# Optimization experiments

Hardware: AMD Instinct MI355X
Metric: run time of the kernel (lower is better)

## Reference

```python
import jax, jax.numpy as jnp
import numpy as np

N = 100000   # nodes
E = 1600000  # edges
G = 512      # graphs in batch
F_IN = 128
H = 128
F_OUT = 1


def setup_inputs() -> dict:
    key = jax.random.key(0)
    ks = jax.random.split(key, 12)
    x = jax.random.normal(ks[0], (N, F_IN), dtype=jnp.float32)
    src = jax.random.randint(ks[1], (E,), 0, N, dtype=jnp.int32)
    dst = jax.random.randint(ks[2], (E,), 0, N, dtype=jnp.int32)
    node2graph = jnp.sort(jax.random.randint(ks[3], (N,), 0, G, dtype=jnp.int32))
    s_in = 1.0 / np.sqrt(F_IN)
    s_h = 1.0 / np.sqrt(H)
    W0 = jax.random.normal(ks[4], (F_IN, H), dtype=jnp.float32) * s_in
    b0 = jnp.zeros((H,), dtype=jnp.float32)
    W1 = jax.random.normal(ks[5], (H, H), dtype=jnp.float32) * s_h
    b1 = jnp.zeros((H,), dtype=jnp.float32)
    W2 = jax.random.normal(ks[6], (H, H), dtype=jnp.float32) * s_h
    b2 = jnp.zeros((H,), dtype=jnp.float32)
    Wm1 = jax.random.normal(ks[7], (H, H), dtype=jnp.float32) * s_h
    bm1 = jnp.zeros((H,), dtype=jnp.float32)
    Wm2 = jax.random.normal(ks[8], (H, F_OUT), dtype=jnp.float32) * s_h
    bm2 = jnp.zeros((F_OUT,), dtype=jnp.float32)
    return {"x": x, "src": src, "dst": dst, "node2graph": node2graph,
            "W0": W0, "b0": b0, "W1": W1, "b1": b1, "W2": W2, "b2": b2,
            "Wm1": Wm1, "bm1": bm1, "Wm2": Wm2, "bm2": bm2}


def _degree_norms(src, dst):
    ones = jnp.ones((E,), dtype=jnp.float32)
    out_deg = jax.ops.segment_sum(ones, src, num_segments=N)
    in_deg = jax.ops.segment_sum(ones, dst, num_segments=N)
    norm_out = jax.lax.rsqrt(jnp.maximum(out_deg, 1.0))  # [N]
    norm_in = jax.lax.rsqrt(jnp.maximum(in_deg, 1.0))    # [N]
    return norm_out, norm_in


def _graph_conv(x, src, dst, norm_out, norm_in, W, b):
    # DGL GraphConv, norm='both', in_feats <= out_feats path:
    # aggregate normalized src features, then linear + activation.
    xs = x * norm_out[:, None]
    msg = xs[src]                                         # [E, H] gather
    agg = jax.ops.segment_sum(msg, dst, num_segments=N)   # [N, H] scatter-add
    agg = agg * norm_in[:, None]
    return jax.nn.relu(agg @ W + b)


def reference(x, src, dst, node2graph, W0, b0, W1, b1, W2, b2, Wm1, bm1, Wm2, bm2):
    norm_out, norm_in = _degree_norms(src, dst)
    h = _graph_conv(x, src, dst, norm_out, norm_in, W0, b0)
    h = _graph_conv(h, src, dst, norm_out, norm_in, W1, b1)
    h = _graph_conv(h, src, dst, norm_out, norm_in, W2, b2)
    # sum_nodes readout per graph
    g = jax.ops.segment_sum(h, node2graph, num_segments=G)  # [G, H]
    # MLP head: Linear -> ReLU -> Linear
    return jax.nn.relu(g @ Wm1 + bm1) @ Wm2 + bm2           # [G, 1]
```

## Files before the change

### kernel.cpp

```cpp
#include <hip/hip_runtime.h>

#define NN 100000
#define NE 1600000
#define NG 512
#define HD 128

#define NBK 196
#define CHUNK 5120
#define NC 313
#define LH (2 * NBK * NC)

typedef _Float16 half4 __attribute__((ext_vector_type(4)));
typedef _Float16 h8 __attribute__((ext_vector_type(8)));
typedef float f32x4 __attribute__((ext_vector_type(4)));

__global__ __launch_bounds__(256) void k_hist(const int* __restrict__ src,
                                              const int* __restrict__ dst,
                                              int* __restrict__ H) {
    __shared__ int hd[NBK], hs[NBK];
    int c = blockIdx.x;
    for (int i = threadIdx.x; i < NBK; i += 256) { hd[i] = 0; hs[i] = 0; }
    __syncthreads();
    int e0 = c * CHUNK;
    int e1 = e0 + CHUNK; if (e1 > NE) e1 = NE;
    for (int e = e0 + threadIdx.x; e < e1; e += 256) {
        atomicAdd(&hd[dst[e] >> 9], 1);
        atomicAdd(&hs[src[e] >> 9], 1);
    }
    __syncthreads();
    for (int i = threadIdx.x; i < NBK; i += 256) {
        H[i * NC + c] = hd[i];
        H[NBK * NC + i * NC + c] = hs[i];
    }
}

__global__ __launch_bounds__(256) void k_scan1g(int* __restrict__ H,
                                                int* __restrict__ bsum, int L) {
    __shared__ int s[256];
    int i = blockIdx.x * 256 + threadIdx.x;
    int v = (i < L) ? H[i] : 0;
    s[threadIdx.x] = v;
    __syncthreads();
    for (int off = 1; off < 256; off <<= 1) {
        int t = (threadIdx.x >= off) ? s[threadIdx.x - off] : 0;
        __syncthreads();
        s[threadIdx.x] += t;
        __syncthreads();
    }
    if (i < L) H[i] = s[threadIdx.x] - v;
    if (threadIdx.x == 255) bsum[blockIdx.x] = s[255];
}

__global__ __launch_bounds__(512) void k_scan2(int* __restrict__ bsum, int nb) {
    __shared__ int s[512];
    int v = (threadIdx.x < nb) ? bsum[threadIdx.x] : 0;
    s[threadIdx.x] = v;
    __syncthreads();
    for (int off = 1; off < 512; off <<= 1) {
        int t = (threadIdx.x >= off) ? s[threadIdx.x - off] : 0;
        __syncthreads();
        s[threadIdx.x] += t;
        __syncthreads();
    }
    if (threadIdx.x < nb) bsum[threadIdx.x] = s[threadIdx.x] - v;
}

__global__ __launch_bounds__(256) void k_scan3g(int* __restrict__ H,
                                                const int* __restrict__ bsum, int L) {
    int i = blockIdx.x * 256 + threadIdx.x;
    if (i < L) H[i] += bsum[i >> 8];
}

__global__ __launch_bounds__(256) void k_scatter(const int* __restrict__ src,
                                                 const int* __restrict__ dst,
                                                 const int* __restrict__ H,
                                                 int2* __restrict__ dpart,
                                                 int* __restrict__ spart) {
    __shared__ int cd[NBK], cs[NBK];
    int c = blockIdx.x;
    for (int i = threadIdx.x; i < NBK; i += 256) {
        cd[i] = H[i * NC + c];
        cs[i] = H[NBK * NC + i * NC + c] - NE;
    }
    __syncthreads();
    int e0 = c * CHUNK;
    int e1 = e0 + CHUNK; if (e1 > NE) e1 = NE;
    for (int e = e0 + threadIdx.x; e < e1; e += 256) {
        int s = src[e], d = dst[e];
        int pd = atomicAdd(&cd[d >> 9], 1);
        dpart[pd] = make_int2(s, d);
        int ps = atomicAdd(&cs[s >> 9], 1);
        spart[ps] = s;
    }
}

__global__ __launch_bounds__(256) void k_bucket(const int2* __restrict__ dpart,
                                                const int* __restrict__ spart,
                                                const int* __restrict__ H,
                                                int* __restrict__ offs,
                                                int* __restrict__ csr,
                                                float* __restrict__ ni,
                                                float* __restrict__ no) {
    __shared__ int deg[512];
    __shared__ int cur[512];
    __shared__ int tmp[256];
    int b = blockIdx.x;
    bool isDst = (b < NBK);
    int bb = isDst ? b : b - NBK;
    int start, end;
    if (isDst) {
        start = H[bb * NC];
        end = (bb + 1 < NBK) ? H[(bb + 1) * NC] : NE;
    } else {
        start = H[NBK * NC + bb * NC] - NE;
        end = (bb + 1 < NBK) ? H[NBK * NC + (bb + 1) * NC] - NE : NE;
    }
    for (int i = threadIdx.x; i < 512; i += 256) deg[i] = 0;
    __syncthreads();
    if (isDst) {
        for (int i = start + threadIdx.x; i < end; i += 256)
            atomicAdd(&deg[dpart[i].y & 511], 1);
    } else {
        for (int i = start + threadIdx.x; i < end; i += 256)
            atomicAdd(&deg[spart[i] & 511], 1);
    }
    __syncthreads();
    int vb = bb * 512;
    if (!isDst) {
        for (int i = threadIdx.x; i < 512; i += 256) {
            int v = vb + i;
            if (v < NN) no[v] = rsqrtf(fmaxf((float)deg[i], 1.0f));
        }
        return;
    }
    int t = threadIdx.x;
    int a0 = deg[2 * t], a1 = deg[2 * t + 1];
    int pair = a0 + a1;
    tmp[t] = pair;
    __syncthreads();
    for (int off = 1; off < 256; off <<= 1) {
        int v2 = (t >= off) ? tmp[t - off] : 0;
        __syncthreads();
        tmp[t] += v2;
        __syncthreads();
    }
    int ex = tmp[t] - pair;
    cur[2 * t] = start + ex;
    cur[2 * t + 1] = start + ex + a0;
    __syncthreads();
    for (int i = threadIdx.x; i < 512; i += 256) {
        int v = vb + i;
        if (v < NN) {
            offs[v] = cur[i];
            ni[v] = rsqrtf(fmaxf((float)deg[i], 1.0f));
        }
    }
    if (b == NBK - 1 && threadIdx.x == 0) offs[NN] = NE;
    __syncthreads();
    for (int i = start + threadIdx.x; i < end; i += 256) {
        int2 e = dpart[i];
        int p = atomicAdd(&cur[e.y & 511], 1);
        csr[p] = e.x;
    }
}

__global__ __launch_bounds__(256) void k_castw(const float* __restrict__ W0,
                                               const float* __restrict__ W1,
                                               const float* __restrict__ W2,
                                               _Float16* __restrict__ Bt) {
    int i = blockIdx.x * 256 + threadIdx.x;
    if (i >= 3 * 16384) return;
    int w = i >> 14;
    int rem = i & 16383;
    int n = rem >> 7;
    int k = rem & 127;
    const float* W = (w == 0) ? W0 : ((w == 1) ? W1 : W2);
    Bt[i] = (_Float16)W[k * 128 + n];
}

template <typename TA>
__global__ __launch_bounds__(256) void k_gemm_mfma(const TA* __restrict__ A,
                                                   const _Float16* __restrict__ Bt,
                                                   const float* __restrict__ no,
                                                   _Float16* __restrict__ Zh,
                                                   int nrows) {
    __shared__ _Float16 Bs[128 * 136];
    int tid = threadIdx.x;
    {
        const h8* B8 = (const h8*)Bt;
        h8* Bs8 = (h8*)Bs;
        for (int i = tid; i < 2048; i += 256) {
            int n = i >> 4, c = i & 15;
            Bs8[n * 17 + c] = B8[i];
        }
    }

    int wave = tid >> 6;
    int lane = tid & 63;
    int m16 = lane & 15;
    int quad = lane >> 4;
    int rowbase = blockIdx.x * 64 + wave * 16;
    int row = rowbase + m16;
    bool valid = row < nrows;

    h8 afrag[4];
    if (valid) {
        if constexpr (sizeof(TA) == 2) {
            const h8* Arow = (const h8*)(A + (size_t)row * 128);
#pragma unroll
            for (int kk = 0; kk < 4; kk++) afrag[kk] = Arow[kk * 4 + quad];
        } else {
            const float4* Arow = (const float4*)(A + (size_t)row * 128);
#pragma unroll
            for (int kk = 0; kk < 4; kk++) {
                float4 lo = Arow[kk * 8 + quad * 2];
                float4 hi = Arow[kk * 8 + quad * 2 + 1];
                h8 a;
                a[0] = (_Float16)lo.x; a[1] = (_Float16)lo.y;
                a[2] = (_Float16)lo.z; a[3] = (_Float16)lo.w;
                a[4] = (_Float16)hi.x; a[5] = (_Float16)hi.y;
                a[6] = (_Float16)hi.z; a[7] = (_Float16)hi.w;
                afrag[kk] = a;
            }
        }
    } else {
#pragma unroll
        for (int kk = 0; kk < 4; kk++) {
            h8 a;
#pragma unroll
            for (int j = 0; j < 8; j++) a[j] = (_Float16)0.f;
            afrag[kk] = a;
        }
    }

    __syncthreads();

    f32x4 acc[8];
#pragma unroll
    for (int nt = 0; nt < 8; nt++) acc[nt] = (f32x4){0.f, 0.f, 0.f, 0.f};

    const h8* Bs8 = (const h8*)Bs;
#pragma unroll
    for (int nt = 0; nt < 8; nt++) {
        const h8* Bp = Bs8 + (size_t)(nt * 16 + m16) * 17;
#pragma unroll
        for (int kk = 0; kk < 4; kk++) {
            acc[nt] = __builtin_amdgcn_mfma_f32_16x16x32_f16(afrag[kk], Bp[kk * 4 + quad],
                                                             acc[nt], 0, 0, 0);
        }
    }

    float nor[4];
#pragma unroll
    for (int r = 0; r < 4; r++) {
        int grow = rowbase + quad * 4 + r;
        nor[r] = (grow < nrows) ? no[grow] : 0.f;
    }

    __syncthreads();
    {
        int lr0 = wave * 16 + quad * 4;
#pragma unroll
        for (int nt = 0; nt < 8; nt++) {
#pragma unroll
            for (int r = 0; r < 4; r++) {
                Bs[(size_t)(lr0 + r) * 136 + nt * 16 + m16] =
                    (_Float16)(acc[nt][r] * nor[r]);
            }
        }
    }
    __syncthreads();

    int blockrow0 = blockIdx.x * 64;
    for (int i = tid; i < 1024; i += 256) {
        int r = i >> 4, cch = i & 15;
        int grow = blockrow0 + r;
        if (grow < nrows) {
            h8 val = *(const h8*)&Bs[(size_t)r * 136 + cch * 8];
            *(h8*)&Zh[(size_t)grow * 128 + cch * 8] = val;
        }
    }
}

__global__ __launch_bounds__(128) void k_agg(const h8* __restrict__ Zh,
                                             const int* __restrict__ offs,
                                             const int* __restrict__ csr,
                                             const float* __restrict__ ni,
                                             const float* __restrict__ b,
                                             h8* __restrict__ H16) {
    int v = blockIdx.x * 8 + (threadIdx.x >> 4);
    int c = threadIdx.x & 15;
    int s = offs[v];
    int e = offs[v + 1];
    float a0[8], a1[8];
#pragma unroll
    for (int j = 0; j < 8; j++) { a0[j] = 0.f; a1[j] = 0.f; }
    int i = s;
    for (; i + 4 <= e; i += 4) {
        int u0 = csr[i];
        int u1 = csr[i + 1];
        int u2 = csr[i + 2];
        int u3 = csr[i + 3];
        h8 z0 = Zh[(size_t)u0 * 16 + c];
        h8 z1 = Zh[(size_t)u1 * 16 + c];
        h8 z2 = Zh[(size_t)u2 * 16 + c];
        h8 z3 = Zh[(size_t)u3 * 16 + c];
#pragma unroll
        for (int j = 0; j < 8; j++) {
            a0[j] += (float)z0[j] + (float)z1[j];
            a1[j] += (float)z2[j] + (float)z3[j];
        }
    }
    for (; i < e; i++) {
        int u = csr[i];
        h8 z = Zh[(size_t)u * 16 + c];
#pragma unroll
        for (int j = 0; j < 8; j++) a0[j] += (float)z[j];
    }
    float niv = ni[v];
    const float* bb = b + c * 8;
    h8 r;
#pragma unroll
    for (int j = 0; j < 8; j++)
        r[j] = (_Float16)fmaxf((a0[j] + a1[j]) * niv + bb[j], 0.f);
    H16[(size_t)v * 16 + c] = r;
}

__global__ __launch_bounds__(128) void k_readout(const h8* __restrict__ H8,
                                                 const int* __restrict__ n2g,
                                                 float* __restrict__ g) {
    __shared__ float red[128 * 8];
    int gi = blockIdx.x;
    int t = threadIdx.x;
    int slot = t >> 4;
    int c = t & 15;

    int lo = 0, hi = NN;
    while (lo < hi) { int mid = (lo + hi) >> 1; if (n2g[mid] < gi) lo = mid + 1; else hi = mid; }
    int s = lo;
    hi = NN;
    while (lo < hi) { int mid = (lo + hi) >> 1; if (n2g[mid] < gi + 1) lo = mid + 1; else hi = mid; }
    int e = lo;

    float acc[8];
#pragma unroll
    for (int j = 0; j < 8; j++) acc[j] = 0.f;
    for (int v = s + slot; v < e; v += 8) {
        h8 z = H8[(size_t)v * 16 + c];
#pragma unroll
        for (int j = 0; j < 8; j++) acc[j] += (float)z[j];
    }
#pragma unroll
    for (int j = 0; j < 8; j++) red[t * 8 + j] = acc[j];
    __syncthreads();
    for (int off = 4; off >= 1; off >>= 1) {
        if (slot < off) {
#pragma unroll
            for (int j = 0; j < 8; j++)
                red[t * 8 + j] += red[(t + off * 16) * 8 + j];
        }
        __syncthreads();
    }
    if (slot == 0) {
#pragma unroll
        for (int j = 0; j < 8; j++)
            g[gi * 128 + c * 8 + j] = red[t * 8 + j];
    }
}

__global__ __launch_bounds__(128) void k_head(const float* __restrict__ g,
                                              const float* __restrict__ Wm1,
                                              const float* __restrict__ bm1,
                                              const float* __restrict__ Wm2,
                                              const float* __restrict__ bm2,
                                              float* __restrict__ out) {
    __shared__ float gs[128];
    __shared__ float red[128];
    int gi = blockIdx.x;
    int f = threadIdx.x;
    gs[f] = g[gi * 128 + f];
    __syncthreads();
    float acc = bm1[f];
    for (int k = 0; k < 128; k++) acc += gs[k] * Wm1[k * 128 + f];
    float h1 = fmaxf(acc, 0.f);
    red[f] = h1 * Wm2[f];
    __syncthreads();
    for (int s2 = 64; s2 > 0; s2 >>= 1) {
        if (f < s2) red[f] += red[f + s2];
        __syncthreads();
    }
    if (f == 0) out[gi] = red[0] + bm2[0];
}

extern "C" void kernel_launch(void* const* d_in, const int* in_sizes, int n_in,
                              void* d_out, int out_size, void* d_ws, size_t ws_size,
                              hipStream_t stream) {
    const float* x   = (const float*)d_in[0];
    const int*   src = (const int*)d_in[1];
    const int*   dst = (const int*)d_in[2];
    const int*   n2g = (const int*)d_in[3];
    const float* W0  = (const float*)d_in[4];
    const float* b0  = (const float*)d_in[5];
    const float* W1  = (const float*)d_in[6];
    const float* b1  = (const float*)d_in[7];
    const float* W2  = (const float*)d_in[8];
    const float* b2  = (const float*)d_in[9];
    const float* Wm1 = (const float*)d_in[10];
    const float* bm1 = (const float*)d_in[11];
    const float* Wm2 = (const float*)d_in[12];
    const float* bm2 = (const float*)d_in[13];
    float* out = (float*)d_out;

    char* p = (char*)d_ws;
    auto carve = [&](size_t bytes) -> char* {
        char* r = p;
        p += (bytes + 255) & ~(size_t)255;
        return r;
    };
    _Float16* zh  = (_Float16*)carve((size_t)NN * HD * 2);
    _Float16* h16 = (_Float16*)carve((size_t)NN * HD * 2);
    _Float16* Bt  = (_Float16*)carve((size_t)3 * 128 * 128 * 2);
    float* no     = (float*)carve((size_t)NN * 4);
    float* ni     = (float*)carve((size_t)NN * 4);
    int*   offs   = (int*)carve((size_t)(NN + 1) * 4);
    int*   csr    = (int*)carve((size_t)NE * 4);
    int*   Hh     = (int*)carve((size_t)LH * 4);
    int*   bsum   = (int*)carve((size_t)512 * 4);
    int2*  dpart  = (int2*)carve((size_t)NE * 8);
    int*   spart  = (int*)carve((size_t)NE * 4);
    float* g      = (float*)carve((size_t)NG * HD * 4);

    k_castw<<<(3 * 16384 + 255) / 256, 256, 0, stream>>>(W0, W1, W2, Bt);

    int scan_blocks = (LH + 255) / 256;
    k_hist<<<NC, 256, 0, stream>>>(src, dst, Hh);
    k_scan1g<<<scan_blocks, 256, 0, stream>>>(Hh, bsum, LH);
    k_scan2<<<1, 512, 0, stream>>>(bsum, scan_blocks);
    k_scan3g<<<scan_blocks, 256, 0, stream>>>(Hh, bsum, LH);
    k_scatter<<<NC, 256, 0, stream>>>(src, dst, Hh, dpart, spart);
    k_bucket<<<2 * NBK, 256, 0, stream>>>(dpart, spart, Hh, offs, csr, ni, no);

    int gemm_blocks = (NN + 63) / 64;

    k_gemm_mfma<float><<<gemm_blocks, 256, 0, stream>>>(x, Bt, no, zh, NN);
    k_agg<<<NN / 8, 128, 0, stream>>>((const h8*)zh, offs, csr, ni, b0, (h8*)h16);
    k_gemm_mfma<_Float16><<<gemm_blocks, 256, 0, stream>>>(h16, Bt + 16384, no, zh, NN);
    k_agg<<<NN / 8, 128, 0, stream>>>((const h8*)zh, offs, csr, ni, b1, (h8*)h16);
    k_gemm_mfma<_Float16><<<gemm_blocks, 256, 0, stream>>>(h16, Bt + 32768, no, zh, NN);
    k_agg<<<NN / 8, 128, 0, stream>>>((const h8*)zh, offs, csr, ni, b2, (h8*)h16);

    k_readout<<<NG, 128, 0, stream>>>((const h8*)h16, n2g, g);
    k_head<<<NG, 128, 0, stream>>>(g, Wm1, bm1, Wm2, bm2, out);
}
```

Measured before the change: 417.6 us.

## Pack partition entries into narrower ints and persist B fragments in GEMM registers

The scatter/bucket stage now packs each dst-partition entry into one 32-bit int (17-bit source plus 9-bit local dst), and stores the src partition as 16-bit local indices. This halves or more the traffic of the CSR-build intermediates. The GEMM kernel loads all B fragments into registers once and loops over four 64-row tiles per block. Each wave writes its own rows through LDS without block-wide syncs, so B staging is amortised over more rows. The cost is much higher register pressure (128 h8 B regs per lane), which may reduce occupancy.

Measured after the change: 420.5 us. About the same (+0.7%).

```diff
diff --git a/kernel.cpp b/kernel.cpp
--- a/kernel.cpp
+++ b/kernel.cpp
@@ -74,8 +74,8 @@
 __global__ __launch_bounds__(256) void k_scatter(const int* __restrict__ src,
                                                  const int* __restrict__ dst,
                                                  const int* __restrict__ H,
-                                                 int2* __restrict__ dpart,
-                                                 int* __restrict__ spart) {
+                                                 int* __restrict__ dpart,
+                                                 unsigned short* __restrict__ spart) {
     __shared__ int cd[NBK], cs[NBK];
     int c = blockIdx.x;
     for (int i = threadIdx.x; i < NBK; i += 256) {
@@ -88,14 +88,14 @@
     for (int e = e0 + threadIdx.x; e < e1; e += 256) {
         int s = src[e], d = dst[e];
         int pd = atomicAdd(&cd[d >> 9], 1);
-        dpart[pd] = make_int2(s, d);
+        dpart[pd] = s | ((d & 511) << 17);
         int ps = atomicAdd(&cs[s >> 9], 1);
-        spart[ps] = s;
-    }
-}
-
-__global__ __launch_bounds__(256) void k_bucket(const int2* __restrict__ dpart,
-                                                const int* __restrict__ spart,
+        spart[ps] = (unsigned short)(s & 511);
+    }
+}
+
+__global__ __launch_bounds__(256) void k_bucket(const int* __restrict__ dpart,
+                                                const unsigned short* __restrict__ spart,
                                                 const int* __restrict__ H,
                                                 int* __restrict__ offs,
                                                 int* __restrict__ csr,
@@ -119,10 +119,10 @@
     __syncthreads();
     if (isDst) {
         for (int i = start + threadIdx.x; i < end; i += 256)
-            atomicAdd(&deg[dpart[i].y & 511], 1);
+            atomicAdd(&deg[(dpart[i] >> 17) & 511], 1);
     } else {
         for (int i = start + threadIdx.x; i < end; i += 256)
-            atomicAdd(&deg[spart[i] & 511], 1);
+            atomicAdd(&deg[spart[i]], 1);
     }
     __syncthreads();
     int vb = bb * 512;
@@ -158,9 +158,9 @@
     if (b == NBK - 1 && threadIdx.x == 0) offs[NN] = NE;
     __syncthreads();
     for (int i = start + threadIdx.x; i < end; i += 256) {
-        int2 e = dpart[i];
-        int p = atomicAdd(&cur[e.y & 511], 1);
-        csr[p] = e.x;
+        int pk = dpart[i];
+        int p = atomicAdd(&cur[(pk >> 17) & 511], 1);
+        csr[p] = pk & 0x1FFFF;
     }
 }
 
@@ -194,71 +194,79 @@
             Bs8[n * 17 + c] = B8[i];
         }
     }
+    __syncthreads();
 
     int wave = tid >> 6;
     int lane = tid & 63;
     int m16 = lane & 15;
     int quad = lane >> 4;
-    int rowbase = blockIdx.x * 64 + wave * 16;
-    int row = rowbase + m16;
-    bool valid = row < nrows;
-
-    h8 afrag[4];
-    if (valid) {
-        if constexpr (sizeof(TA) == 2) {
-            const h8* Arow = (const h8*)(A + (size_t)row * 128);
-#pragma unroll
-            for (int kk = 0; kk < 4; kk++) afrag[kk] = Arow[kk * 4 + quad];
+
+    h8 breg[8][4];
+    {
+        const h8* Bs8 = (const h8*)Bs;
+#pragma unroll
+        for (int nt = 0; nt < 8; nt++) {
+            const h8* Bp = Bs8 + (size_t)(nt * 16 + m16) * 17;
+#pragma unroll
+            for (int kk = 0; kk < 4; kk++) breg[nt][kk] = Bp[kk * 4 + quad];
+        }
+    }
+    __syncthreads();
+
+#pragma unroll 1
+    for (int t = 0; t < 4; t++) {
+        int rowbase = blockIdx.x * 256 + t * 64 + wave * 16;
+        int row = rowbase + m16;
+        bool valid = row < nrows;
+
+        h8 afrag[4];
+        if (valid) {
+            if constexpr (sizeof(TA) == 2) {
+                const h8* Arow = (const h8*)(A + (size_t)row * 128);
+#pragma unroll
+                for (int kk = 0; kk < 4; kk++) afrag[kk] = Arow[kk * 4 + quad];
+            } else {
+                const float4* Arow = (const float4*)(A + (size_t)row * 128);
+#pragma unroll
+                for (int kk = 0; kk < 4; kk++) {
+                    float4 lo = Arow[kk * 8 + quad * 2];
+                    float4 hi = Arow[kk * 8 + quad * 2 + 1];
+                    h8 a;
+                    a[0] = (_Float16)lo.x; a[1] = (_Float16)lo.y;
+                    a[2] = (_Float16)lo.z; a[3] = (_Float16)lo.w;
+                    a[4] = (_Float16)hi.x; a[5] = (_Float16)hi.y;
+                    a[6] = (_Float16)hi.z; a[7] = (_Float16)hi.w;
+                    afrag[kk] = a;
+                }
+            }
         } else {
-            const float4* Arow = (const float4*)(A + (size_t)row * 128);
 #pragma unroll
             for (int kk = 0; kk < 4; kk++) {
-                float4 lo = Arow[kk * 8 + quad * 2];
-                float4 hi = Arow[kk * 8 + quad * 2 + 1];
                 h8 a;
-                a[0] = (_Float16)lo.x; a[1] = (_Float16)lo.y;
-                a[2] = (_Float16)lo.z; a[3] = (_Float16)lo.w;
-                a[4] = (_Float16)hi.x; a[5] = (_Float16)hi.y;
-                a[6] = (_Float16)hi.z; a[7] = (_Float16)hi.w;
+#pragma unroll
+                for (int j = 0; j < 8; j++) a[j] = (_Float16)0.f;
                 afrag[kk] = a;
             }
         }
-    } else {
-#pragma unroll
-        for (int kk = 0; kk < 4; kk++) {
-            h8 a;
-#pragma unroll
-            for (int j = 0; j < 8; j++) a[j] = (_Float16)0.f;
-            afrag[kk] = a;
-        }
-    }
-
-    __syncthreads();
-
-    f32x4 acc[8];
-#pragma unroll
-    for (int nt = 0; nt < 8; nt++) acc[nt] = (f32x4){0.f, 0.f, 0.f, 0.f};
-
-    const h8* Bs8 = (const h8*)Bs;
-#pragma unroll
-    for (int nt = 0; nt < 8; nt++) {
-        const h8* Bp = Bs8 + (size_t)(nt * 16 + m16) * 17;
-#pragma unroll
-        for (int kk = 0; kk < 4; kk++) {
-            acc[nt] = __builtin_amdgcn_mfma_f32_16x16x32_f16(afrag[kk], Bp[kk * 4 + quad],
-                                                             acc[nt], 0, 0, 0);
-        }
-    }
-
-    float nor[4];
-#pragma unroll
-    for (int r = 0; r < 4; r++) {
-        int grow = rowbase + quad * 4 + r;
-        nor[r] = (grow < nrows) ? no[grow] : 0.f;
-    }
-
-    __syncthreads();
-    {
+
+        f32x4 acc[8];
+#pragma unroll
+        for (int nt = 0; nt < 8; nt++) acc[nt] = (f32x4){0.f, 0.f, 0.f, 0.f};
+#pragma unroll
+        for (int nt = 0; nt < 8; nt++) {
+#pragma unroll
+            for (int kk = 0; kk < 4; kk++) {
+                acc[nt] = __builtin_amdgcn_mfma_f32_16x16x32_f16(afrag[kk], breg[nt][kk],
+                                                                 acc[nt], 0, 0, 0);
+            }
+        }
+
+        float nor[4];
+#pragma unroll
+        for (int r = 0; r < 4; r++) {
+            int grow = rowbase + quad * 4 + r;
+            nor[r] = (grow < nrows) ? no[grow] : 0.f;
+        }
         int lr0 = wave * 16 + quad * 4;
 #pragma unroll
         for (int nt = 0; nt < 8; nt++) {
@@ -268,16 +276,15 @@
                     (_Float16)(acc[nt][r] * nor[r]);
             }
         }
-    }
-    __syncthreads();
-
-    int blockrow0 = blockIdx.x * 64;
-    for (int i = tid; i < 1024; i += 256) {
-        int r = i >> 4, cch = i & 15;
-        int grow = blockrow0 + r;
-        if (grow < nrows) {
-            h8 val = *(const h8*)&Bs[(size_t)r * 136 + cch * 8];
-            *(h8*)&Zh[(size_t)grow * 128 + cch * 8] = val;
+#pragma unroll
+        for (int p2 = 0; p2 < 4; p2++) {
+            int r2 = p2 * 4 + (lane >> 4);
+            int cch = lane & 15;
+            int grow = rowbase + r2;
+            if (grow < nrows) {
+                h8 val = *(const h8*)&Bs[(size_t)(wave * 16 + r2) * 136 + cch * 8];
+                *(h8*)&Zh[(size_t)grow * 128 + cch * 8] = val;
+            }
         }
     }
 }
@@ -426,8 +433,8 @@
     int*   csr    = (int*)carve((size_t)NE * 4);
     int*   Hh     = (int*)carve((size_t)LH * 4);
     int*   bsum   = (int*)carve((size_t)512 * 4);
-    int2*  dpart  = (int2*)carve((size_t)NE * 8);
-    int*   spart  = (int*)carve((size_t)NE * 4);
+    int*   dpart  = (int*)carve((size_t)NE * 4);
+    unsigned short* spart = (unsigned short*)carve((size_t)NE * 2);
     float* g      = (float*)carve((size_t)NG * HD * 4);
 
     k_castw<<<(3 * 16384 + 255) / 256, 256, 0, stream>>>(W0, W1, W2, Bt);
@@ -440,7 +447,7 @@
     k_scatter<<<NC, 256, 0, stream>>>(src, dst, Hh, dpart, spart);
     k_bucket<<<2 * NBK, 256, 0, stream>>>(dpart, spart, Hh, offs, csr, ni, no);
 
-    int gemm_blocks = (NN + 63) / 64;
+    int gemm_blocks = (NN + 255) / 256;
 
     k_gemm_mfma<float><<<gemm_blocks, 256, 0, stream>>>(x, Bt, no, zh, NN);
     k_agg<<<NN / 8, 128, 0, stream>>>((const h8*)zh, offs, csr, ni, b0, (h8*)h16);
```
